# Optimization experiments

Measured on AMD Instinct MI355X. Metric: run time of the kernel, lower is better.

Reference implementation:

```python
import jax, jax.numpy as jnp
import numpy as np

L = (7, 5, 5, 5, 5)            # num_quantized_values (all odd -> exact product codebook)
LATENT_DIM = len(L)
MAX_SEQ_LEN = 2048
LATENT_SEQ_LEN = 1024
CODEBOOK_SIZE = int(np.prod(L))  # 4375


def build_codebook():
    # Matches build_codebook_recursive: dim 0 varies slowest ('ij' meshgrid + ravel).
    ranges = [jnp.arange(-(l // 2), l // 2 + 1, dtype=jnp.int32) for l in L]
    grids = jnp.meshgrid(*ranges, indexing='ij')
    return jnp.stack([g.ravel() for g in grids], axis=-1)  # [K, D] int32


def setup_inputs() -> dict:
    key = jax.random.key(0)
    k1, k2, k3 = jax.random.split(key, 3)
    B, S, D = 16, MAX_SEQ_LEN, 1024
    x = jax.random.normal(k1, (B, S, D), dtype=jnp.float32)
    W_enc = jax.random.normal(k2, (D, LATENT_DIM), dtype=jnp.float32) / np.sqrt(D)
    W_dec = jax.random.normal(k3, (LATENT_DIM, D), dtype=jnp.float32) / np.sqrt(LATENT_DIM)
    return {"x": x, "W_enc": W_enc, "W_dec": W_dec}


def reference(x, W_enc, W_dec):
    B, S, _ = x.shape
    codebook = build_codebook()                                   # [K, D_lat]
    half = jnp.array([l // 2 for l in L], dtype=jnp.float32)      # (L/2).int()

    # encode: stand-in linear encoder, then zero tokens past latent_seq_len
    h = jnp.einsum('bsd,de->bse', x, W_enc)                        # [B,S,D_lat]
    mask = (jnp.arange(S) < LATENT_SEQ_LEN)[None, :, None]
    h = h * mask
    z_e = h.reshape(-1, LATENT_DIM)                                # [N, D_lat]

    # quantize: FSQ tanh squash + round with straight-through estimator
    z_e_sq = half * jnp.tanh(z_e)
    z_q = jnp.round(z_e_sq)
    z = jax.lax.stop_gradient(z_q - z_e_sq) + z_e_sq

    # brute-force codebook index lookup: [N,1,D] == [K,D] -> all -> argmax
    matches = jnp.all(z.astype(jnp.int32)[:, None, :] == codebook[None], axis=-1)  # [N,K]
    idx = jnp.argmax(matches, axis=1)                              # [N]

    # codebook usage (fresh zero-initialized usage buffer)
    used = jnp.zeros((CODEBOOK_SIZE,), dtype=jnp.float32).at[idx].set(1.0)
    unique = jnp.sum(used)
    usage = (unique + (CODEBOOK_SIZE - unique) * jnp.exp(jnp.float32(-1.0))) / CODEBOOK_SIZE

    # decode: stand-in linear decoder
    z3 = z.reshape(-1, MAX_SEQ_LEN, LATENT_DIM)                    # [B, num_latents, D_lat]
    x_out = jnp.einsum('bse,ed->bsd', z3, W_dec)                   # [B,S,D]
    percent_masked = jnp.float32(0.0)

    return x_out, z_e, z_q, usage, unique.astype(jnp.int32), percent_masked
```

## Files before the change

kernel.cpp:

```cpp
#include <hip/hip_runtime.h>

#define MAX_SEQ   2048
#define LAT_SEQ   1024
#define DIM       1024
#define DLAT      5
#define K_CB      4375
#define ZERO_IDX  2187

typedef float vf4 __attribute__((ext_vector_type(4)));

__device__ __forceinline__ void nt_store4(float* p, vf4 v) {
    __builtin_nontemporal_store(v, (vf4*)p);
}

__global__ __launch_bounds__(256) void fsq_main(
    const float* __restrict__ x,
    const float* __restrict__ Wenc,
    const float* __restrict__ Wdec,
    float* __restrict__ xout,
    float* __restrict__ ze,
    float* __restrict__ zq,
    int*   __restrict__ used)
{
    __shared__ float wencT[DLAT * DIM];

    const int tid  = threadIdx.x;
    const int wave = tid >> 6;
    const int lane = tid & 63;
    const int u0   = (blockIdx.x * 4 + wave) * 2;

    int t[2];  long long row[2], rowm[2];
    #pragma unroll
    for (int p = 0; p < 2; ++p) {
        const int u = u0 + p;
        const int b = u >> 10, s = u & 1023;
        t[p]    = b * MAX_SEQ + s;
        row[p]  = (long long)t[p] * DIM;
        rowm[p] = row[p] + (long long)LAT_SEQ * DIM;
    }

    float4 v[2][4];
    #pragma unroll
    for (int p = 0; p < 2; ++p)
        #pragma unroll
        for (int q = 0; q < 4; ++q)
            v[p][q] = *(const float4*)(x + row[p] + q * 256 + lane * 4);

    const vf4 z4 = {0.f, 0.f, 0.f, 0.f};
    #pragma unroll
    for (int p = 0; p < 2; ++p) {
        #pragma unroll
        for (int q = 0; q < 4; ++q)
            nt_store4(xout + rowm[p] + q * 256 + lane * 4, z4);
        if (lane < DLAT) {
            const int tm = t[p] + LAT_SEQ;
            ze[tm * DLAT + lane] = 0.f;
            zq[tm * DLAT + lane] = 0.f;
        }
    }

    #pragma unroll
    for (int m = 0; m < 20; ++m) {
        const int k = tid + 256 * m;
        const int e = k >> 10, d = k & 1023;
        wencT[k] = Wenc[d * DLAT + e];
    }
    __syncthreads();

    float acc[2][DLAT] = {};
    #pragma unroll
    for (int q = 0; q < 4; ++q) {
        const int c0 = q * 256 + lane * 4;
        #pragma unroll
        for (int e = 0; e < DLAT; ++e) {
            const float4 w = *(const float4*)(wencT + e * DIM + c0);
            #pragma unroll
            for (int p = 0; p < 2; ++p)
                acc[p][e] += v[p][q].x * w.x + v[p][q].y * w.y
                           + v[p][q].z * w.z + v[p][q].w * w.w;
        }
    }
    #pragma unroll
    for (int p = 0; p < 2; ++p)
        #pragma unroll
        for (int e = 0; e < DLAT; ++e) {
            float a = acc[p][e];
            #pragma unroll
            for (int o = 32; o > 0; o >>= 1) a += __shfl_xor(a, o, 64);
            acc[p][e] = a;
        }

    const float halfv[DLAT] = {3.f, 2.f, 2.f, 2.f, 2.f};
    float zqv[2][DLAT];
    #pragma unroll
    for (int p = 0; p < 2; ++p) {
        int ci[DLAT];
        #pragma unroll
        for (int e = 0; e < DLAT; ++e) {
            const float zsq = halfv[e] * tanhf(acc[p][e]);
            zqv[p][e] = rintf(zsq);
            ci[e]     = (int)zqv[p][e];
        }
        if (lane < DLAT) {
            ze[t[p] * DLAT + lane] = acc[p][lane];
            zq[t[p] * DLAT + lane] = zqv[p][lane];
        }
        if (lane == 0) {
            const int idx = ((((ci[0] + 3) * 5 + (ci[1] + 2)) * 5 + (ci[2] + 2)) * 5
                              + (ci[3] + 2)) * 5 + (ci[4] + 2);
            used[idx] = 1;
        }
    }

    #pragma unroll
    for (int q = 0; q < 4; ++q) {
        const int c0 = q * 256 + lane * 4;
        vf4 o[2] = {{0.f,0.f,0.f,0.f}, {0.f,0.f,0.f,0.f}};
        #pragma unroll
        for (int e = 0; e < DLAT; ++e) {
            const float4 w = *(const float4*)(Wdec + e * DIM + c0);
            #pragma unroll
            for (int p = 0; p < 2; ++p) {
                o[p].x += zqv[p][e] * w.x; o[p].y += zqv[p][e] * w.y;
                o[p].z += zqv[p][e] * w.z; o[p].w += zqv[p][e] * w.w;
            }
        }
        #pragma unroll
        for (int p = 0; p < 2; ++p)
            nt_store4(xout + row[p] + c0, o[p]);
    }
}

__global__ void finalize(const int* __restrict__ used, float* __restrict__ scal) {
    __shared__ int sh[256];
    const int t = threadIdx.x;
    int sum = 0;
    for (int i = t; i < K_CB; i += 256) sum += used[i];
    sh[t] = sum;
    __syncthreads();
    for (int o = 128; o > 0; o >>= 1) {
        if (t < o) sh[t] += sh[t + o];
        __syncthreads();
    }
    if (t == 0) {
        const float uniq  = (float)sh[0] + (used[ZERO_IDX] ? 0.f : 1.f);
        const float usage = (uniq + ((float)K_CB - uniq) * expf(-1.0f)) / (float)K_CB;
        scal[0] = usage;
        scal[1] = uniq;
        scal[2] = 0.0f;
    }
}

extern "C" void kernel_launch(void* const* d_in, const int* in_sizes, int n_in,
                              void* d_out, int out_size, void* d_ws, size_t ws_size,
                              hipStream_t stream) {
    const float* x    = (const float*)d_in[0];
    const float* Wenc = (const float*)d_in[1];
    const float* Wdec = (const float*)d_in[2];

    float* out  = (float*)d_out;
    float* xout = out;
    float* ze   = out + 33554432;
    float* zq   = ze + 163840;
    float* scal = zq + 163840;

    int* used = (int*)d_ws;

    hipMemsetAsync(used, 0, K_CB * sizeof(int), stream);
    fsq_main<<<2048, 256, 0, stream>>>(x, Wenc, Wdec, xout, ze, zq, used);
    finalize<<<1, 256, 0, stream>>>(used, scal);
}
```

Measured before the change: 44.91 us.

## Drop LDS transpose of Wenc and move codebook usage into finalize kernel

The main kernel now reads Wenc directly from global memory in its native [D,5] layout, each lane loading 5 contiguous float4s. This removes the shared-memory transpose staging and its block barrier. The global used buffer, its memset launch and the per-token atomic-free writes are gone. The finalize kernel instead rebuilds a shared-memory bitmap by re-reading zq for the 16384 unmasked tokens with 1024 threads. The trade is one fewer launch and less main-kernel work against a larger serial single-block finalize step.

```diff
diff --git a/kernel.cpp b/kernel.cpp
--- a/kernel.cpp
+++ b/kernel.cpp
@@ -19,14 +19,10 @@
     const float* __restrict__ Wdec,
     float* __restrict__ xout,
     float* __restrict__ ze,
-    float* __restrict__ zq,
-    int*   __restrict__ used)
+    float* __restrict__ zq)
 {
-    __shared__ float wencT[DLAT * DIM];
-
-    const int tid  = threadIdx.x;
-    const int wave = tid >> 6;
-    const int lane = tid & 63;
+    const int wave = threadIdx.x >> 6;
+    const int lane = threadIdx.x & 63;
     const int u0   = (blockIdx.x * 4 + wave) * 2;
 
     int t[2];  long long row[2], rowm[2];
@@ -59,25 +55,23 @@
         }
     }
 
-    #pragma unroll
-    for (int m = 0; m < 20; ++m) {
-        const int k = tid + 256 * m;
-        const int e = k >> 10, d = k & 1023;
-        wencT[k] = Wenc[d * DLAT + e];
-    }
-    __syncthreads();
-
     float acc[2][DLAT] = {};
     #pragma unroll
     for (int q = 0; q < 4; ++q) {
         const int c0 = q * 256 + lane * 4;
+        float4 w4[5];
+        const float4* wp = (const float4*)(Wenc + c0 * DLAT);
         #pragma unroll
-        for (int e = 0; e < DLAT; ++e) {
-            const float4 w = *(const float4*)(wencT + e * DIM + c0);
+        for (int m = 0; m < 5; ++m) w4[m] = wp[m];
+        const float* w = (const float*)w4;
+        #pragma unroll
+        for (int p = 0; p < 2; ++p) {
+            const float vv[4] = {v[p][q].x, v[p][q].y, v[p][q].z, v[p][q].w};
             #pragma unroll
-            for (int p = 0; p < 2; ++p)
-                acc[p][e] += v[p][q].x * w.x + v[p][q].y * w.y
-                           + v[p][q].z * w.z + v[p][q].w * w.w;
+            for (int j = 0; j < 4; ++j)
+                #pragma unroll
+                for (int e = 0; e < DLAT; ++e)
+                    acc[p][e] += vv[j] * w[j * DLAT + e];
         }
     }
     #pragma unroll
@@ -94,56 +88,69 @@
     float zqv[2][DLAT];
     #pragma unroll
     for (int p = 0; p < 2; ++p) {
-        int ci[DLAT];
         #pragma unroll
-        for (int e = 0; e < DLAT; ++e) {
-            const float zsq = halfv[e] * tanhf(acc[p][e]);
-            zqv[p][e] = rintf(zsq);
-            ci[e]     = (int)zqv[p][e];
-        }
+        for (int e = 0; e < DLAT; ++e)
+            zqv[p][e] = rintf(halfv[e] * tanhf(acc[p][e]));
         if (lane < DLAT) {
             ze[t[p] * DLAT + lane] = acc[p][lane];
             zq[t[p] * DLAT + lane] = zqv[p][lane];
-        }
-        if (lane == 0) {
-            const int idx = ((((ci[0] + 3) * 5 + (ci[1] + 2)) * 5 + (ci[2] + 2)) * 5
-                              + (ci[3] + 2)) * 5 + (ci[4] + 2);
-            used[idx] = 1;
         }
     }
 
     #pragma unroll
     for (int q = 0; q < 4; ++q) {
         const int c0 = q * 256 + lane * 4;
-        vf4 o[2] = {{0.f,0.f,0.f,0.f}, {0.f,0.f,0.f,0.f}};
+        float4 w[DLAT];
         #pragma unroll
-        for (int e = 0; e < DLAT; ++e) {
-            const float4 w = *(const float4*)(Wdec + e * DIM + c0);
+        for (int e = 0; e < DLAT; ++e)
+            w[e] = *(const float4*)(Wdec + e * DIM + c0);
+        #pragma unroll
+        for (int p = 0; p < 2; ++p) {
+            vf4 o = {0.f, 0.f, 0.f, 0.f};
             #pragma unroll
-            for (int p = 0; p < 2; ++p) {
-                o[p].x += zqv[p][e] * w.x; o[p].y += zqv[p][e] * w.y;
-                o[p].z += zqv[p][e] * w.z; o[p].w += zqv[p][e] * w.w;
+            for (int e = 0; e < DLAT; ++e) {
+                o.x += zqv[p][e] * w[e].x; o.y += zqv[p][e] * w[e].y;
+                o.z += zqv[p][e] * w[e].z; o.w += zqv[p][e] * w[e].w;
             }
+            nt_store4(xout + row[p] + c0, o);
         }
-        #pragma unroll
-        for (int p = 0; p < 2; ++p)
-            nt_store4(xout + row[p] + c0, o[p]);
     }
 }
 
-__global__ void finalize(const int* __restrict__ used, float* __restrict__ scal) {
-    __shared__ int sh[256];
-    const int t = threadIdx.x;
+__global__ __launch_bounds__(1024) void finalize(
+    const float* __restrict__ zq, float* __restrict__ scal)
+{
+    __shared__ unsigned char bm[K_CB];
+    __shared__ int sh[16];
+    const int tid = threadIdx.x;
+
+    for (int i = tid; i < K_CB; i += 1024) bm[i] = 0;
+    __syncthreads();
+
+    for (int u = tid; u < 16384; u += 1024) {
+        const int t = (u >> 10) * MAX_SEQ + (u & 1023);
+        const float* z = zq + (long long)t * DLAT;
+        const int c0 = (int)z[0], c1 = (int)z[1], c2 = (int)z[2],
+                  c3 = (int)z[3], c4 = (int)z[4];
+        const int idx = ((((c0 + 3) * 5 + (c1 + 2)) * 5 + (c2 + 2)) * 5
+                          + (c3 + 2)) * 5 + (c4 + 2);
+        bm[idx] = 1;
+    }
+    __syncthreads();
+    if (tid == 0) bm[ZERO_IDX] = 1;
+    __syncthreads();
+
     int sum = 0;
-    for (int i = t; i < K_CB; i += 256) sum += used[i];
-    sh[t] = sum;
+    for (int i = tid; i < K_CB; i += 1024) sum += bm[i];
+    #pragma unroll
+    for (int o = 32; o > 0; o >>= 1) sum += __shfl_xor(sum, o, 64);
+    if ((tid & 63) == 0) sh[tid >> 6] = sum;
     __syncthreads();
-    for (int o = 128; o > 0; o >>= 1) {
-        if (t < o) sh[t] += sh[t + o];
-        __syncthreads();
-    }
-    if (t == 0) {
-        const float uniq  = (float)sh[0] + (used[ZERO_IDX] ? 0.f : 1.f);
+    if (tid == 0) {
+        int tot = 0;
+        #pragma unroll
+        for (int wv = 0; wv < 16; ++wv) tot += sh[wv];
+        const float uniq  = (float)tot;
         const float usage = (uniq + ((float)K_CB - uniq) * expf(-1.0f)) / (float)K_CB;
         scal[0] = usage;
         scal[1] = uniq;
@@ -164,9 +171,8 @@
     float* zq   = ze + 163840;
     float* scal = zq + 163840;
 
-    int* used = (int*)d_ws;
+    (void)d_ws; (void)ws_size;
 
-    hipMemsetAsync(used, 0, K_CB * sizeof(int), stream);
-    fsq_main<<<2048, 256, 0, stream>>>(x, Wenc, Wdec, xout, ze, zq, used);
-    finalize<<<1, 256, 0, stream>>>(used, scal);
+    fsq_main<<<2048, 256, 0, stream>>>(x, Wenc, Wdec, xout, ze, zq);
+    finalize<<<1, 1024, 0, stream>>>(zq, scal);
 }
```

Result: slower. 60.53 us (+34.8%).
